# Kernel optimization log

Hardware: AMD Instinct MI355X
Metric: run time of the kernel (lower is better)

The kernel has to match this reference:

```python
import jax, jax.numpy as jnp
import numpy as np

B, DIM, H, W = 128, 640, 10, 10
M = H * W


def setup_inputs() -> dict:
    key = jax.random.key(0)
    x = jax.random.normal(key, (B, DIM, M), dtype=jnp.float32)
    # learned temperature parameter, init = log(1 / (2*h*w)), shape (1, 1)
    t = jnp.log(1.0 / (2 * H * W) * jnp.ones((1, 1), dtype=jnp.float32))
    return {"x": x, "t": t}


def reference(x, t):
    # x: [B, dim, M], t: [1, 1] temperature (log-scale)
    dim = x.shape[1]
    # Gram matrix x x^T: [B, dim, dim]
    xxT = jnp.einsum('bdm,bem->bde', x, x)
    # I_M.bmm(x_pow2*I) and (x_pow2*I).bmm(I_M) are just diagonal broadcasts
    d = jnp.diagonal(xxT, axis1=1, axis2=2)  # [B, dim]
    dcov = d[:, None, :] + d[:, :, None] - 2.0 * xxT
    dcov = jnp.maximum(dcov, 1e-4)
    dcov = jnp.sqrt(jnp.exp(t) * dcov + 1e-5)
    # double centering: dcov.bmm(I_M)/dim == row means, I_M.bmm(dcov)/dim == col means
    row_mean = jnp.mean(dcov, axis=2, keepdims=True)   # [B, dim, 1]
    col_mean = jnp.mean(dcov, axis=1, keepdims=True)   # [B, 1, dim]
    tot_mean = jnp.mean(dcov, axis=(1, 2), keepdims=True)  # [B, 1, 1]
    out = dcov - row_mean - col_mean + tot_mean
    return out.reshape(out.shape[0], dim * dim)
```

## Files before the change

### kernel.cpp

```cpp
#include <hip/hip_runtime.h>
#include <cmath>

#define NB    128
#define DIM_  640
#define MM    100
#define XHR   128
#define LDSH  128
#define TFS   68
#define TTS   66
#define RSS   34
#define CSS   10

#define NWG   (NB * 55)
#define CPX   (NWG / 8)

typedef _Float16 half8 __attribute__((ext_vector_type(8)));
typedef float f32x4 __attribute__((ext_vector_type(4)));

#define FSQRT(x) __builtin_amdgcn_sqrtf(x)

__device__ inline void decode_bp(int bid, int& b, int& p) {
    const int dec = (bid & 7) * CPX + (bid >> 3);
    b = dec / 55;
    p = dec - b * 55;
}

__global__ __launch_bounds__(256) void prep_xh(const float* __restrict__ x,
                                               _Float16* __restrict__ xh,
                                               float* __restrict__ d,
                                               float* __restrict__ rmz) {
    if (blockIdx.x < 321) {
        const int z = blockIdx.x * 256 + threadIdx.x;
        if (z < 82048) rmz[z] = 0.f;
    }
    const int row  = blockIdx.x * 4 + (threadIdx.x >> 6);
    const int lane = threadIdx.x & 63;
    const float* xr = x + (size_t)row * MM;
    float2 v = make_float2(0.f, 0.f);
    if (lane < 50) v = *(const float2*)(xr + 2 * lane);
    const _Float16 h0 = (_Float16)v.x, h1 = (_Float16)v.y;
    const float a0 = (float)h0, a1 = (float)h1;
    float acc = a0 * a0 + a1 * a1;
    union { _Float16 h[2]; unsigned u; } pk;
    pk.h[0] = h0; pk.h[1] = h1;
    *(unsigned*)(xh + (size_t)row * XHR + 2 * lane) = pk.u;
    #pragma unroll
    for (int off = 32; off; off >>= 1) acc += __shfl_down(acc, off, 64);
    if (lane == 0) d[row] = acc;
}

__device__ inline void stage_xh_async(const _Float16* __restrict__ src,
                                      _Float16* lds, int tid) {
    #pragma unroll
    for (int i = 0; i < 4; ++i) {
        const int c   = tid + i * 256;
        const int row = c >> 4;
        const int m   = (c & 15) ^ (row & 7);
        __builtin_amdgcn_global_load_lds(
            (const __attribute__((address_space(1))) unsigned int*)(const void*)(src + (size_t)row * XHR + m * 8),
            (__attribute__((address_space(3))) unsigned int*)(void*)(lds + (size_t)c * 8),
            16, 0, 0);
    }
}

__device__ inline half8 frg(const _Float16* lds, int row, int kk, int quad) {
    const int slot = (kk * 4 + quad) ^ (row & 7);
    return *(const half8*)(lds + row * LDSH + slot * 8);
}

__global__ __launch_bounds__(256, 4) void bdc_sums(
        const _Float16* __restrict__ xh, const float* __restrict__ d,
        const float* __restrict__ t, float* __restrict__ rm,
        float* __restrict__ tot) {
    __shared__ alignas(16) _Float16 As[64 * LDSH];
    __shared__ alignas(16) _Float16 Bs[64 * LDSH];
    float* rsum = (float*)As;
    float* csum = (float*)As + 64 * RSS;

    int b, p;
    decode_bp(blockIdx.x, b, p);
    int it = 0, rem = p;
    while (rem >= 10 - it) { rem -= 10 - it; ++it; }
    const int jt = it + rem;
    const bool diag = (it == jt);

    const int tid = threadIdx.x;
    const int wave = tid >> 6;
    const int lane = tid & 63;
    const int l16  = lane & 15;
    const int quad = lane >> 4;
    const int rowhalf = wave >> 1;
    const int colhalf = wave & 1;

    const _Float16* xb = xh + (size_t)b * DIM_ * XHR;
    stage_xh_async(xb + (size_t)(it * 64) * XHR, As, tid);
    if (!diag) stage_xh_async(xb + (size_t)(jt * 64) * XHR, Bs, tid);

    const float expt = __expf(t[0]);
    const float* db = d + b * DIM_;
    const int rbase = it * 64 + rowhalf * 32;
    const int cbase = jt * 64 + colhalf * 32;
    float dr[2][4];
    #pragma unroll
    for (int ti = 0; ti < 2; ++ti)
        #pragma unroll
        for (int r = 0; r < 4; ++r)
            dr[ti][r] = db[rbase + ti * 16 + quad * 4 + r];
    const float dcv[2] = { db[cbase + l16], db[cbase + 16 + l16] };

    __syncthreads();

    const _Float16* Bp = diag ? As : Bs;
    f32x4 acc[2][2] = {};
    #pragma unroll
    for (int kk = 0; kk < 4; ++kk) {
        half8 a0 = frg(As, rowhalf * 32 + l16,      kk, quad);
        half8 a1 = frg(As, rowhalf * 32 + 16 + l16, kk, quad);
        half8 b0 = frg(Bp, colhalf * 32 + l16,      kk, quad);
        half8 b1 = frg(Bp, colhalf * 32 + 16 + l16, kk, quad);
        acc[0][0] = __builtin_amdgcn_mfma_f32_16x16x32_f16(a0, b0, acc[0][0], 0, 0, 0);
        acc[0][1] = __builtin_amdgcn_mfma_f32_16x16x32_f16(a0, b1, acc[0][1], 0, 0, 0);
        acc[1][0] = __builtin_amdgcn_mfma_f32_16x16x32_f16(a1, b0, acc[1][0], 0, 0, 0);
        acc[1][1] = __builtin_amdgcn_mfma_f32_16x16x32_f16(a1, b1, acc[1][1], 0, 0, 0);
    }

    float s2[2][4];
    float cp0 = 0.f, cp1 = 0.f;
    #pragma unroll
    for (int ti = 0; ti < 2; ++ti) {
        #pragma unroll
        for (int r = 0; r < 4; ++r) {
            const int gi = rbase + ti * 16 + quad * 4 + r;
            float raw0 = dr[ti][r] + dcv[0] - 2.0f * acc[ti][0][r];
            raw0 = (gi == cbase + l16) ? 1e-4f : fmaxf(raw0, 1e-4f);
            const float v0 = FSQRT(expt * raw0 + 1e-5f);
            float raw1 = dr[ti][r] + dcv[1] - 2.0f * acc[ti][1][r];
            raw1 = (gi == cbase + 16 + l16) ? 1e-4f : fmaxf(raw1, 1e-4f);
            const float v1 = FSQRT(expt * raw1 + 1e-5f);
            s2[ti][r] = v0 + v1;
            cp0 += v0; cp1 += v1;
        }
    }

    __syncthreads();

    #pragma unroll
    for (int ti = 0; ti < 2; ++ti)
        #pragma unroll
        for (int r = 0; r < 4; ++r)
            rsum[(rowhalf * 32 + ti * 16 + quad * 4 + r) * RSS + colhalf * 16 + l16] = s2[ti][r];
    csum[(colhalf * 32 + l16) * CSS + rowhalf * 4 + quad]      = cp0;
    csum[(colhalf * 32 + 16 + l16) * CSS + rowhalf * 4 + quad] = cp1;

    __syncthreads();

    if (tid < 64) {
        float rt = 0.f;
        const float2* rp = (const float2*)(rsum + tid * RSS);
        #pragma unroll
        for (int k = 0; k < 16; ++k) { const float2 u = rp[k]; rt += u.x + u.y; }
        atomicAdd(&rm[b * DIM_ + it * 64 + tid], rt);
        float ts = rt;
        #pragma unroll
        for (int off = 1; off < 64; off <<= 1) ts += __shfl_xor(ts, off, 64);
        if (tid == 0) atomicAdd(&tot[b], diag ? ts : 2.0f * ts);
    } else if (tid < 128 && !diag) {
        const int c = tid - 64;
        float ct = 0.f;
        #pragma unroll
        for (int s = 0; s < 8; ++s) ct += csum[c * CSS + s];
        atomicAdd(&rm[b * DIM_ + jt * 64 + c], ct);
    }
}

__global__ __launch_bounds__(256) void bdc_out(
        const _Float16* __restrict__ xh, const float* __restrict__ d,
        const float* __restrict__ t, const float* __restrict__ rm,
        const float* __restrict__ tot_g, float* __restrict__ out) {
    __shared__ alignas(16) char uni[34304];
    _Float16* As = (_Float16*)uni;
    _Float16* Bs = (_Float16*)(uni + 16384);
    float* Tf = (float*)uni;
    float* Tt = (float*)(uni + 17408);
    __shared__ float rm_i[64];
    __shared__ float rm_j[64];

    int b, p;
    decode_bp(blockIdx.x, b, p);
    int it = 0, rem = p;
    while (rem >= 10 - it) { rem -= 10 - it; ++it; }
    const int jt = it + rem;
    const bool diag = (it == jt);

    const int tid  = threadIdx.x;
    const int wave = tid >> 6;
    const int lane = tid & 63;
    const int l16  = lane & 15;
    const int quad = lane >> 4;
    const int rowhalf = wave >> 1;
    const int colhalf = wave & 1;

    const _Float16* xb = xh + (size_t)b * DIM_ * XHR;
    stage_xh_async(xb + (size_t)(it * 64) * XHR, As, tid);
    if (!diag) stage_xh_async(xb + (size_t)(jt * 64) * XHR, Bs, tid);

    const float* rmg = rm + (size_t)b * DIM_;
    if (tid < 64)       rm_i[tid]      = rmg[it * 64 + tid]        * (1.0f / 640.0f);
    else if (tid < 128) rm_j[tid - 64] = rmg[jt * 64 + (tid - 64)] * (1.0f / 640.0f);
    const float tot = tot_g[b] * (1.0f / 409600.0f);

    const float expt = __expf(t[0]);
    const float* db = d + b * DIM_;
    const int rbase = it * 64 + rowhalf * 32;
    const int cbase = jt * 64 + colhalf * 32;
    float dr[2][4];
    #pragma unroll
    for (int ti = 0; ti < 2; ++ti)
        #pragma unroll
        for (int r = 0; r < 4; ++r)
            dr[ti][r] = db[rbase + ti * 16 + quad * 4 + r];
    const float dcv[2] = { db[cbase + l16], db[cbase + 16 + l16] };

    __syncthreads();

    const _Float16* Bp = diag ? As : Bs;
    f32x4 acc[2][2] = {};
    #pragma unroll
    for (int kk = 0; kk < 4; ++kk) {
        half8 a0 = frg(As, rowhalf * 32 + l16,      kk, quad);
        half8 a1 = frg(As, rowhalf * 32 + 16 + l16, kk, quad);
        half8 b0 = frg(Bp, colhalf * 32 + l16,      kk, quad);
        half8 b1 = frg(Bp, colhalf * 32 + 16 + l16, kk, quad);
        acc[0][0] = __builtin_amdgcn_mfma_f32_16x16x32_f16(a0, b0, acc[0][0], 0, 0, 0);
        acc[0][1] = __builtin_amdgcn_mfma_f32_16x16x32_f16(a0, b1, acc[0][1], 0, 0, 0);
        acc[1][0] = __builtin_amdgcn_mfma_f32_16x16x32_f16(a1, b0, acc[1][0], 0, 0, 0);
        acc[1][1] = __builtin_amdgcn_mfma_f32_16x16x32_f16(a1, b1, acc[1][1], 0, 0, 0);
    }

    float o[2][4][2];
    #pragma unroll
    for (int ti = 0; ti < 2; ++ti)
        #pragma unroll
        for (int r = 0; r < 4; ++r) {
            const int rowl = rowhalf * 32 + ti * 16 + quad * 4 + r;
            const int gi = it * 64 + rowl;
            const float rowterm = tot - rm_i[rowl];
            #pragma unroll
            for (int tj = 0; tj < 2; ++tj) {
                const int coll = colhalf * 32 + tj * 16 + l16;
                const int gj = jt * 64 + coll;
                float raw = dr[ti][r] + dcv[tj] - 2.0f * acc[ti][tj][r];
                raw = (gi == gj) ? 1e-4f : fmaxf(raw, 1e-4f);
                o[ti][r][tj] = FSQRT(expt * raw + 1e-5f) + rowterm - rm_j[coll];
            }
        }

    __syncthreads();

    #pragma unroll
    for (int ti = 0; ti < 2; ++ti)
        #pragma unroll
        for (int r = 0; r < 4; ++r) {
            const int rowl = rowhalf * 32 + ti * 16 + quad * 4 + r;
            #pragma unroll
            for (int tj = 0; tj < 2; ++tj) {
                const int coll = colhalf * 32 + tj * 16 + l16;
                Tf[rowl * TFS + coll] = o[ti][r][tj];
                if (!diag)
                    Tt[coll * TTS + (rowl ^ ((l16 & 3) << 2))] = o[ti][r][tj];
            }
        }

    __syncthreads();

    float* ob = out + (size_t)b * DIM_ * DIM_;
    #pragma unroll
    for (int k4 = 0; k4 < 4; ++k4) {
        const int w  = tid + k4 * 256;
        const int rr = w >> 4;
        const int c4 = (w & 15) * 4;
        const f32x4 v = *(const f32x4*)(&Tf[rr * TFS + c4]);
        __builtin_nontemporal_store(v, (f32x4*)(ob + (size_t)(it * 64 + rr) * DIM_ + jt * 64 + c4));
    }
    if (!diag) {
        #pragma unroll
        for (int k4 = 0; k4 < 4; ++k4) {
            const int w  = tid + k4 * 256;
            const int rr = w >> 4;
            const int c4 = (w & 15) * 4;
            const int cc = c4 ^ ((rr & 3) << 2);
            const float2 p0 = *(const float2*)(&Tt[rr * TTS + cc]);
            const float2 p1 = *(const float2*)(&Tt[rr * TTS + cc + 2]);
            const f32x4 v = { p0.x, p0.y, p1.x, p1.y };
            __builtin_nontemporal_store(v, (f32x4*)(ob + (size_t)(jt * 64 + rr) * DIM_ + it * 64 + c4));
        }
    }
}

extern "C" void kernel_launch(void* const* d_in, const int* in_sizes, int n_in,
                              void* d_out, int out_size, void* d_ws, size_t ws_size,
                              hipStream_t stream) {
    const float* x = (const float*)d_in[0];
    const float* t = (const float*)d_in[1];
    float* out = (float*)d_out;

    char* ws = (char*)d_ws;
    _Float16* xh = (_Float16*)ws;
    float*    d  = (float*)(ws + 20971520);
    float*    rm = (float*)(ws + 20971520 + 327680);
    float*    tot= (float*)(ws + 20971520 + 2 * 327680);

    prep_xh<<<dim3(NB * DIM_ / 4), dim3(256), 0, stream>>>(x, xh, d, rm);
    bdc_sums<<<dim3(NWG), dim3(256), 0, stream>>>(xh, d, t, rm, tot);
    bdc_out<<<dim3(NWG), dim3(256), 0, stream>>>(xh, d, t, rm, tot, out);
}
```

Baseline: 271.8 us.

## Fuse sums and output kernels with per-batch atomic spin barrier

Merges the row-sum pass and the output pass into one kernel. Each workgroup keeps its computed distance tile in registers, publishes its row and column sums, then waits on a per-batch atomic counter until all 55 tiles of that batch have contributed. This removes the second Gram MFMA pass, the repeated sqrt, the second staging of the half-precision inputs and one kernel launch. The counter lives in the zeroed workspace: the zeroing loop's bounds check is dropped so it now also clears the counters. The cost is spin-waiting, lower occupancy (launch bound 3), and a reliance on all tiles of a batch being co-resident; if they are not, the kernel can deadlock.

```diff
diff --git a/kernel.cpp b/kernel.cpp
--- a/kernel.cpp
+++ b/kernel.cpp
@@ -29,10 +29,8 @@
                                                _Float16* __restrict__ xh,
                                                float* __restrict__ d,
                                                float* __restrict__ rmz) {
-    if (blockIdx.x < 321) {
-        const int z = blockIdx.x * 256 + threadIdx.x;
-        if (z < 82048) rmz[z] = 0.f;
-    }
+    if (blockIdx.x < 321)
+        rmz[blockIdx.x * 256 + threadIdx.x] = 0.f;
     const int row  = blockIdx.x * 4 + (threadIdx.x >> 6);
     const int lane = threadIdx.x & 63;
     const float* xr = x + (size_t)row * MM;
@@ -68,14 +66,20 @@
     return *(const half8*)(lds + row * LDSH + slot * 8);
 }
 
-__global__ __launch_bounds__(256, 4) void bdc_sums(
+__global__ __launch_bounds__(256, 3) void bdc_fused(
         const _Float16* __restrict__ xh, const float* __restrict__ d,
         const float* __restrict__ t, float* __restrict__ rm,
-        float* __restrict__ tot) {
-    __shared__ alignas(16) _Float16 As[64 * LDSH];
-    __shared__ alignas(16) _Float16 Bs[64 * LDSH];
-    float* rsum = (float*)As;
-    float* csum = (float*)As + 64 * RSS;
+        float* __restrict__ tot_g, unsigned* __restrict__ cnt,
+        float* __restrict__ out) {
+    __shared__ alignas(16) char uni[34304];
+    _Float16* As = (_Float16*)uni;
+    _Float16* Bs = (_Float16*)(uni + 16384);
+    float* rsum = (float*)uni;
+    float* csum = (float*)uni + 64 * RSS;
+    float* Tf = (float*)uni;
+    float* Tt = (float*)(uni + 17408);
+    __shared__ float rm_i[64];
+    __shared__ float rm_j[64];
 
     int b, p;
     decode_bp(blockIdx.x, b, p);
@@ -124,7 +128,7 @@
         acc[1][1] = __builtin_amdgcn_mfma_f32_16x16x32_f16(a1, b1, acc[1][1], 0, 0, 0);
     }
 
-    float s2[2][4];
+    float v[2][4][2];
     float cp0 = 0.f, cp1 = 0.f;
     #pragma unroll
     for (int ti = 0; ti < 2; ++ti) {
@@ -133,12 +137,11 @@
             const int gi = rbase + ti * 16 + quad * 4 + r;
             float raw0 = dr[ti][r] + dcv[0] - 2.0f * acc[ti][0][r];
             raw0 = (gi == cbase + l16) ? 1e-4f : fmaxf(raw0, 1e-4f);
-            const float v0 = FSQRT(expt * raw0 + 1e-5f);
+            v[ti][r][0] = FSQRT(expt * raw0 + 1e-5f);
             float raw1 = dr[ti][r] + dcv[1] - 2.0f * acc[ti][1][r];
             raw1 = (gi == cbase + 16 + l16) ? 1e-4f : fmaxf(raw1, 1e-4f);
-            const float v1 = FSQRT(expt * raw1 + 1e-5f);
-            s2[ti][r] = v0 + v1;
-            cp0 += v0; cp1 += v1;
+            v[ti][r][1] = FSQRT(expt * raw1 + 1e-5f);
+            cp0 += v[ti][r][0]; cp1 += v[ti][r][1];
         }
     }
 
@@ -148,7 +151,8 @@
     for (int ti = 0; ti < 2; ++ti)
         #pragma unroll
         for (int r = 0; r < 4; ++r)
-            rsum[(rowhalf * 32 + ti * 16 + quad * 4 + r) * RSS + colhalf * 16 + l16] = s2[ti][r];
+            rsum[(rowhalf * 32 + ti * 16 + quad * 4 + r) * RSS + colhalf * 16 + l16] =
+                v[ti][r][0] + v[ti][r][1];
     csum[(colhalf * 32 + l16) * CSS + rowhalf * 4 + quad]      = cp0;
     csum[(colhalf * 32 + 16 + l16) * CSS + rowhalf * 4 + quad] = cp1;
 
@@ -163,7 +167,7 @@
         float ts = rt;
         #pragma unroll
         for (int off = 1; off < 64; off <<= 1) ts += __shfl_xor(ts, off, 64);
-        if (tid == 0) atomicAdd(&tot[b], diag ? ts : 2.0f * ts);
+        if (tid == 0) atomicAdd(&tot_g[b], diag ? ts : 2.0f * ts);
     } else if (tid < 128 && !diag) {
         const int c = tid - 64;
         float ct = 0.f;
@@ -171,103 +175,37 @@
         for (int s = 0; s < 8; ++s) ct += csum[c * CSS + s];
         atomicAdd(&rm[b * DIM_ + jt * 64 + c], ct);
     }
-}
-
-__global__ __launch_bounds__(256) void bdc_out(
-        const _Float16* __restrict__ xh, const float* __restrict__ d,
-        const float* __restrict__ t, const float* __restrict__ rm,
-        const float* __restrict__ tot_g, float* __restrict__ out) {
-    __shared__ alignas(16) char uni[34304];
-    _Float16* As = (_Float16*)uni;
-    _Float16* Bs = (_Float16*)(uni + 16384);
-    float* Tf = (float*)uni;
-    float* Tt = (float*)(uni + 17408);
-    __shared__ float rm_i[64];
-    __shared__ float rm_j[64];
-
-    int b, p;
-    decode_bp(blockIdx.x, b, p);
-    int it = 0, rem = p;
-    while (rem >= 10 - it) { rem -= 10 - it; ++it; }
-    const int jt = it + rem;
-    const bool diag = (it == jt);
-
-    const int tid  = threadIdx.x;
-    const int wave = tid >> 6;
-    const int lane = tid & 63;
-    const int l16  = lane & 15;
-    const int quad = lane >> 4;
-    const int rowhalf = wave >> 1;
-    const int colhalf = wave & 1;
-
-    const _Float16* xb = xh + (size_t)b * DIM_ * XHR;
-    stage_xh_async(xb + (size_t)(it * 64) * XHR, As, tid);
-    if (!diag) stage_xh_async(xb + (size_t)(jt * 64) * XHR, Bs, tid);
+
+    __syncthreads();
+
+    if (tid == 0) {
+        __threadfence();
+        atomicAdd(&cnt[b], 1u);
+        while (__hip_atomic_load(&cnt[b], __ATOMIC_ACQUIRE, __HIP_MEMORY_SCOPE_AGENT) < 55u)
+            __builtin_amdgcn_s_sleep(16);
+    }
+    __syncthreads();
 
     const float* rmg = rm + (size_t)b * DIM_;
     if (tid < 64)       rm_i[tid]      = rmg[it * 64 + tid]        * (1.0f / 640.0f);
     else if (tid < 128) rm_j[tid - 64] = rmg[jt * 64 + (tid - 64)] * (1.0f / 640.0f);
-    const float tot = tot_g[b] * (1.0f / 409600.0f);
-
-    const float expt = __expf(t[0]);
-    const float* db = d + b * DIM_;
-    const int rbase = it * 64 + rowhalf * 32;
-    const int cbase = jt * 64 + colhalf * 32;
-    float dr[2][4];
-    #pragma unroll
-    for (int ti = 0; ti < 2; ++ti)
-        #pragma unroll
-        for (int r = 0; r < 4; ++r)
-            dr[ti][r] = db[rbase + ti * 16 + quad * 4 + r];
-    const float dcv[2] = { db[cbase + l16], db[cbase + 16 + l16] };
-
-    __syncthreads();
-
-    const _Float16* Bp = diag ? As : Bs;
-    f32x4 acc[2][2] = {};
-    #pragma unroll
-    for (int kk = 0; kk < 4; ++kk) {
-        half8 a0 = frg(As, rowhalf * 32 + l16,      kk, quad);
-        half8 a1 = frg(As, rowhalf * 32 + 16 + l16, kk, quad);
-        half8 b0 = frg(Bp, colhalf * 32 + l16,      kk, quad);
-        half8 b1 = frg(Bp, colhalf * 32 + 16 + l16, kk, quad);
-        acc[0][0] = __builtin_amdgcn_mfma_f32_16x16x32_f16(a0, b0, acc[0][0], 0, 0, 0);
-        acc[0][1] = __builtin_amdgcn_mfma_f32_16x16x32_f16(a0, b1, acc[0][1], 0, 0, 0);
-        acc[1][0] = __builtin_amdgcn_mfma_f32_16x16x32_f16(a1, b0, acc[1][0], 0, 0, 0);
-        acc[1][1] = __builtin_amdgcn_mfma_f32_16x16x32_f16(a1, b1, acc[1][1], 0, 0, 0);
-    }
-
-    float o[2][4][2];
+    const float totv = tot_g[b] * (1.0f / 409600.0f);
+
+    __syncthreads();
+
     #pragma unroll
     for (int ti = 0; ti < 2; ++ti)
         #pragma unroll
         for (int r = 0; r < 4; ++r) {
             const int rowl = rowhalf * 32 + ti * 16 + quad * 4 + r;
-            const int gi = it * 64 + rowl;
-            const float rowterm = tot - rm_i[rowl];
+            const float rowterm = totv - rm_i[rowl];
             #pragma unroll
             for (int tj = 0; tj < 2; ++tj) {
                 const int coll = colhalf * 32 + tj * 16 + l16;
-                const int gj = jt * 64 + coll;
-                float raw = dr[ti][r] + dcv[tj] - 2.0f * acc[ti][tj][r];
-                raw = (gi == gj) ? 1e-4f : fmaxf(raw, 1e-4f);
-                o[ti][r][tj] = FSQRT(expt * raw + 1e-5f) + rowterm - rm_j[coll];
-            }
-        }
-
-    __syncthreads();
-
-    #pragma unroll
-    for (int ti = 0; ti < 2; ++ti)
-        #pragma unroll
-        for (int r = 0; r < 4; ++r) {
-            const int rowl = rowhalf * 32 + ti * 16 + quad * 4 + r;
-            #pragma unroll
-            for (int tj = 0; tj < 2; ++tj) {
-                const int coll = colhalf * 32 + tj * 16 + l16;
-                Tf[rowl * TFS + coll] = o[ti][r][tj];
+                const float o = v[ti][r][tj] + rowterm - rm_j[coll];
+                Tf[rowl * TFS + coll] = o;
                 if (!diag)
-                    Tt[coll * TTS + (rowl ^ ((l16 & 3) << 2))] = o[ti][r][tj];
+                    Tt[coll * TTS + (rowl ^ ((l16 & 3) << 2))] = o;
             }
         }
 
@@ -279,8 +217,8 @@
         const int w  = tid + k4 * 256;
         const int rr = w >> 4;
         const int c4 = (w & 15) * 4;
-        const f32x4 v = *(const f32x4*)(&Tf[rr * TFS + c4]);
-        __builtin_nontemporal_store(v, (f32x4*)(ob + (size_t)(it * 64 + rr) * DIM_ + jt * 64 + c4));
+        const f32x4 vv = *(const f32x4*)(&Tf[rr * TFS + c4]);
+        __builtin_nontemporal_store(vv, (f32x4*)(ob + (size_t)(it * 64 + rr) * DIM_ + jt * 64 + c4));
     }
     if (!diag) {
         #pragma unroll
@@ -291,8 +229,8 @@
             const int cc = c4 ^ ((rr & 3) << 2);
             const float2 p0 = *(const float2*)(&Tt[rr * TTS + cc]);
             const float2 p1 = *(const float2*)(&Tt[rr * TTS + cc + 2]);
-            const f32x4 v = { p0.x, p0.y, p1.x, p1.y };
-            __builtin_nontemporal_store(v, (f32x4*)(ob + (size_t)(jt * 64 + rr) * DIM_ + it * 64 + c4));
+            const f32x4 vv = { p0.x, p0.y, p1.x, p1.y };
+            __builtin_nontemporal_store(vv, (f32x4*)(ob + (size_t)(jt * 64 + rr) * DIM_ + it * 64 + c4));
         }
     }
 }
@@ -305,12 +243,12 @@
     float* out = (float*)d_out;
 
     char* ws = (char*)d_ws;
-    _Float16* xh = (_Float16*)ws;
-    float*    d  = (float*)(ws + 20971520);
-    float*    rm = (float*)(ws + 20971520 + 327680);
-    float*    tot= (float*)(ws + 20971520 + 2 * 327680);
+    _Float16* xh  = (_Float16*)ws;
+    float*    d   = (float*)(ws + 20971520);
+    float*    rm  = (float*)(ws + 20971520 + 327680);
+    float*    tot = (float*)(ws + 20971520 + 2 * 327680);
+    unsigned* cnt = (unsigned*)(ws + 20971520 + 2 * 327680 + 512);
 
     prep_xh<<<dim3(NB * DIM_ / 4), dim3(256), 0, stream>>>(x, xh, d, rm);
-    bdc_sums<<<dim3(NWG), dim3(256), 0, stream>>>(xh, d, t, rm, tot);
-    bdc_out<<<dim3(NWG), dim3(256), 0, stream>>>(xh, d, t, rm, tot, out);
-}
+    bdc_fused<<<dim3(NWG), dim3(256), 0, stream>>>(xh, d, t, rm, tot, cnt, out);
+}
```

Measured after the change: 693.2 us. 155% more time.
